# Kernel optimization log

Hardware: AMD Instinct MI355X
Metric: run time of the kernel (lower is better)

Reference implementation:

```python
import jax, jax.numpy as jnp
import numpy as np

D_MODEL = 256
N_HEADS = 8
HEAD_DIM = D_MODEL // N_HEADS  # 32
N_LEVELS = 4
N_POINTS = 4
LEVEL_SHAPES = [(100, 100), (50, 50), (25, 25), (13, 13)]
LEVEL_STARTS = [0] + list(np.cumsum([h * w for h, w in LEVEL_SHAPES]))[:-1]
LEN_IN = int(sum(h * w for h, w in LEVEL_SHAPES))  # 13294
BATCH = 2
LEN_Q = LEN_IN  # encoder self-attention


def _offset_bias():
    # faithful to MSDeformAttn._reset_parameters for sampling_offsets bias
    thetas = np.arange(N_HEADS, dtype=np.float32) * (2.0 * np.pi / N_HEADS)
    grid = np.stack([np.cos(thetas), np.sin(thetas)], -1)
    grid = grid / np.abs(grid).max(-1, keepdims=True)
    grid = np.tile(grid.reshape(N_HEADS, 1, 1, 2), (1, N_LEVELS, N_POINTS, 1))
    for i in range(N_POINTS):
        grid[:, :, i, :] *= i + 1
    return jnp.asarray(grid.reshape(-1), dtype=jnp.float32)


def setup_inputs() -> dict:
    key = jax.random.key(0)
    ks = jax.random.split(key, 10)
    s = 1.0 / np.sqrt(D_MODEL)
    inp = {
        "query": jax.random.normal(ks[0], (BATCH, LEN_Q, D_MODEL), jnp.float32),
        "reference_points": jax.random.uniform(ks[1], (BATCH, LEN_Q, N_LEVELS, 2), jnp.float32),
        "input_flatten": jax.random.normal(ks[2], (BATCH, LEN_IN, D_MODEL), jnp.float32),
        "input_spatial_shapes": jnp.asarray(LEVEL_SHAPES, dtype=jnp.int32),
        "W_value": jax.random.normal(ks[3], (D_MODEL, D_MODEL), jnp.float32) * s,
        "b_value": jnp.zeros((D_MODEL,), jnp.float32),
        "W_off": jax.random.normal(ks[4], (D_MODEL, N_HEADS * N_LEVELS * N_POINTS * 2), jnp.float32) * 0.01,
        "b_off": _offset_bias(),
        "W_attn": jax.random.normal(ks[5], (D_MODEL, N_HEADS * N_LEVELS * N_POINTS), jnp.float32) * 0.01,
        "b_attn": jnp.zeros((N_HEADS * N_LEVELS * N_POINTS,), jnp.float32),
        "W_out": jax.random.normal(ks[6], (D_MODEL, D_MODEL), jnp.float32) * s,
        "b_out": jnp.zeros((D_MODEL,), jnp.float32),
    }
    return inp


def _corner(v_t, ix, iy, h, w):
    # v_t: (n, M, h*w, D); ix/iy: (n, M, LqP) int32. Zero padding outside.
    valid = (ix >= 0) & (ix < w) & (iy >= 0) & (iy < h)
    idx = jnp.clip(iy, 0, h - 1) * w + jnp.clip(ix, 0, w - 1)
    g = jnp.take_along_axis(v_t, idx[..., None], axis=2)  # (n, M, LqP, D)
    return g * valid[..., None].astype(v_t.dtype)


def _ms_deform_attn(query, reference_points, input_flatten,
                    W_value, b_value, W_off, b_off, W_attn, b_attn, W_out, b_out):
    n, lq, _ = query.shape
    value = (input_flatten @ W_value + b_value).reshape(n, LEN_IN, N_HEADS, HEAD_DIM)
    offs = (query @ W_off + b_off).reshape(n, lq, N_HEADS, N_LEVELS, N_POINTS, 2)
    aw = jax.nn.softmax(
        (query @ W_attn + b_attn).reshape(n, lq, N_HEADS, N_LEVELS * N_POINTS), axis=-1
    ).reshape(n, lq, N_HEADS, N_LEVELS, N_POINTS)
    # offset_normalizer = (w, h) per level
    norm = jnp.asarray([[w, h] for h, w in LEVEL_SHAPES], dtype=query.dtype)
    loc = reference_points[:, :, None, :, None, :] + offs / norm[None, None, None, :, None, :]

    acc = jnp.zeros((n, N_HEADS, lq, HEAD_DIM), dtype=value.dtype)
    for l, (h, w) in enumerate(LEVEL_SHAPES):
        s0 = LEVEL_STARTS[l]
        v_t = jnp.transpose(value[:, s0:s0 + h * w], (0, 2, 1, 3))  # (n, M, hw, D)
        ll = loc[:, :, :, l]  # (n, lq, M, P, 2) in [0,1]
        # grid_sample bilinear, align_corners=False: pixel = coord*size - 0.5
        x = ll[..., 0] * w - 0.5
        y = ll[..., 1] * h - 0.5
        x0 = jnp.floor(x); y0 = jnp.floor(y)
        tx = x - x0; ty = y - y0
        ix0 = x0.astype(jnp.int32); iy0 = y0.astype(jnp.int32)
        flat = lambda a: jnp.transpose(a, (0, 2, 1, 3)).reshape(n, N_HEADS, lq * N_POINTS)
        ix0f, iy0f = flat(ix0), flat(iy0)
        txf = flat(tx)[..., None]; tyf = flat(ty)[..., None]
        g00 = _corner(v_t, ix0f, iy0f, h, w)
        g01 = _corner(v_t, ix0f + 1, iy0f, h, w)
        g10 = _corner(v_t, ix0f, iy0f + 1, h, w)
        g11 = _corner(v_t, ix0f + 1, iy0f + 1, h, w)
        samp = (g00 * (1 - txf) * (1 - tyf) + g01 * txf * (1 - tyf)
                + g10 * (1 - txf) * tyf + g11 * txf * tyf)
        samp = samp.reshape(n, N_HEADS, lq, N_POINTS, HEAD_DIM)
        wl = jnp.transpose(aw[:, :, :, l], (0, 2, 1, 3))[..., None]  # (n, M, lq, P, 1)
        acc = acc + (samp * wl).sum(axis=3)

    out = jnp.transpose(acc, (0, 2, 1, 3)).reshape(n, lq, D_MODEL)
    return out @ W_out + b_out


def reference(query, reference_points, input_flatten, input_spatial_shapes,
              W_value, b_value, W_off, b_off, W_attn, b_attn, W_out, b_out):
    # input_spatial_shapes carried for signature fidelity; level geometry is static.
    return _ms_deform_attn(query, reference_points, input_flatten,
                           W_value, b_value, W_off, b_off, W_attn, b_attn, W_out, b_out)
```

## Files before the change

### kernel.cpp

```cpp
#include <hip/hip_runtime.h>

#define NH 8
#define HD 32
#define NL 4
#define NP 4
#define DM 256
#define LEN_IN_C 13294
#define LQ_C 13294
#define B_C 2
#define M_TOTAL (B_C * LQ_C)
#define MT_TILES 1662
#define GQ 32
#define QBLKS 831
#define LROWB 1040

typedef __attribute__((ext_vector_type(8))) short short8;
typedef __attribute__((ext_vector_type(4))) float floatx4;

__device__ __forceinline__ unsigned short f2bf(float x) {
    union { float f; unsigned int u; } a; a.f = x;
    unsigned int r = (a.u + 0x7FFFu + ((a.u >> 16) & 1u)) >> 16;
    return (unsigned short)r;
}
__device__ __forceinline__ unsigned short f2h(float x) {
    unsigned int r;
    asm("v_cvt_f16_f32 %0, %1" : "=v"(r) : "v"(x));
    return (unsigned short)r;
}
__device__ __forceinline__ unsigned int cvtpk_bf16(float lo, float hi) {
    unsigned int r;
    asm("v_cvt_pk_bf16_f32 %0, %1, %2" : "=v"(r) : "v"(lo), "v"(hi));
    return r;
}

#define FMAMIX_LO(acc, v, w) \
    asm("v_fma_mix_f32 %0, %1, %2, %0 op_sel_hi:[1,0,0]" : "+v"(acc) : "v"(v), "v"(w))
#define FMAMIX_HI(acc, v, w) \
    asm("v_fma_mix_f32 %0, %1, %2, %0 op_sel:[1,0,0] op_sel_hi:[1,0,0]" : "+v"(acc) : "v"(v), "v"(w))

__device__ __forceinline__ void dma16(const float* g, float* l) {
    __builtin_amdgcn_global_load_lds(
        (const __attribute__((address_space(1))) unsigned int*)(g),
        (__attribute__((address_space(3))) unsigned int*)(l), 16, 0, 0);
}

__device__ __forceinline__ void conv_b_body(const float* __restrict__ W,
                                            unsigned short* __restrict__ Bsw,
                                            int Nsrc, int NTsrc, int NTtotal, int ntOff,
                                            int vblk) {
    const int u = vblk * 256 + threadIdx.x;
    const int lane = u & 63;
    const int unit = u >> 6;
    const int ntl = unit % NTsrc;
    const int kc = unit / NTsrc;
    const int n = ntl * 16 + (lane & 15);
    const int k0 = kc * 32 + (lane >> 4) * 8;
    short8 v;
#pragma unroll
    for (int j = 0; j < 8; ++j)
        v[j] = (short)f2bf(W[(size_t)(k0 + j) * Nsrc + n]);
    ((short8*)Bsw)[(size_t)(kc * NTtotal + ntOff + ntl) * 64 + lane] = v;
}

__global__ __launch_bounds__(256) void conv_weights_kernel(const float* __restrict__ Wv,
                                                           const float* __restrict__ Woff,
                                                           const float* __restrict__ Wattn,
                                                           const float* __restrict__ Wout,
                                                           const float* __restrict__ boff,
                                                           const float* __restrict__ battn,
                                                           unsigned short* __restrict__ BswV,
                                                           unsigned short* __restrict__ BswOA,
                                                           unsigned short* __restrict__ BswO,
                                                           float* __restrict__ fbias,
                                                           unsigned short* __restrict__ value,
                                                           unsigned short* __restrict__ AccSw) {
    const int blk = blockIdx.x;
    if (blk < 32)        conv_b_body(Wv,    BswV,  256, 16, 16, 0,  blk);
    else if (blk < 64)   conv_b_body(Woff,  BswOA, 256, 16, 24, 0,  blk - 32);
    else if (blk < 80)   conv_b_body(Wattn, BswOA, 128,  8, 24, 16, blk - 64);
    else if (blk < 112)  conv_b_body(Wout,  BswO,  256, 16, 16, 0,  blk - 80);
    else if (blk < 114) {
        const int t = (blk - 112) * 256 + threadIdx.x;
        if (t < 384) fbias[t] = (t < 256) ? boff[t] : battn[t - 256];
        else if (t < 416) {
            const int j = t - 384;
            value[-32 + j] = 0;
            value[(size_t)M_TOTAL * 256 + j] = 0;
        }
    } else {
        const int idx = threadIdx.x;
        if (idx < 128) {
            const int kc = idx >> 4;
            const int sub = idx & 15;
            const int lane = (12 + (sub & 3)) + 16 * (sub >> 2);
            const size_t unit = (size_t)(1661 * 8 + kc) * 64 + lane;
            short8 z = (short8){0, 0, 0, 0, 0, 0, 0, 0};
            ((short8*)AccSw)[unit] = z;
        }
    }
}

template <int NT, int OUTMODE>
__device__ __forceinline__ void tile_compute_f32lds(const float* __restrict__ sA,
                                                    const unsigned short* __restrict__ Bsw,
                                                    const float* __restrict__ bias,
                                                    void* __restrict__ Cout, int M, int trow,
                                                    int lane, int wave) {
    constexpr int NTW = NT / 4;
    const int m = lane & 15;
    const int q = lane >> 4;
    const short8* Bu = (const short8*)Bsw;

    floatx4 acc[NTW];
#pragma unroll
    for (int t = 0; t < NTW; ++t) acc[t] = (floatx4){0.f, 0.f, 0.f, 0.f};

#pragma unroll 2
    for (int kc = 0; kc < 8; ++kc) {
        const char* fb = (const char*)sA + m * LROWB + kc * 128 + q * 32;
        const float4 f0 = *(const float4*)fb;
        const float4 f1 = *(const float4*)(fb + 16);
        union { uint4 u; short8 s; } c;
        c.u.x = cvtpk_bf16(f0.x, f0.y); c.u.y = cvtpk_bf16(f0.z, f0.w);
        c.u.z = cvtpk_bf16(f1.x, f1.y); c.u.w = cvtpk_bf16(f1.z, f1.w);
        const short8 a = c.s;
#pragma unroll
        for (int t = 0; t < NTW; ++t) {
            const short8 b = Bu[(size_t)(kc * NT + wave * NTW + t) * 64 + lane];
            acc[t] = __builtin_amdgcn_mfma_f32_16x16x32_bf16(a, b, acc[t], 0, 0, 0);
        }
    }

    const int N = NT * 16;
    const int colq = lane & 15;
    const int rowq = (lane >> 4) * 4;
#pragma unroll
    for (int t = 0; t < NTW; ++t) {
        const int col = (wave * NTW + t) * 16 + colq;
        const float bc = bias[col];
#pragma unroll
        for (int reg = 0; reg < 4; ++reg) {
            const int row = trow + rowq + reg;
            if (row < M) {
                const float v = acc[t][reg] + bc;
                if (OUTMODE == 1) {
                    const int bb = row >= LEN_IN_C;
                    const int pos = row - (bb ? LEN_IN_C : 0);
                    const int hh = col >> 5;
                    const int dd = col & 31;
                    ((unsigned short*)Cout)[((size_t)((bb << 3) + hh) * LEN_IN_C + pos) * 32 + dd] = f2h(v);
                } else {
                    ((float*)Cout)[(size_t)row * N + col] = v;
                }
            }
        }
    }
}

__global__ __launch_bounds__(256) void front_gemm_kernel(const float* __restrict__ inflat,
                                                         const float* __restrict__ query,
                                                         const unsigned short* __restrict__ BswV,
                                                         const unsigned short* __restrict__ BswOA,
                                                         const float* __restrict__ bv,
                                                         const float* __restrict__ fbias,
                                                         unsigned short* __restrict__ value,
                                                         float* __restrict__ fused, int M) {
    __shared__ float sA[16 * LROWB / 4];
    const int tid = threadIdx.x;
    const int lane = tid & 63;
    const int wave = tid >> 6;
    const int x = blockIdx.x;
    const int flavor = x & 1;
    const int trow = (x >> 1) * 16;
    const float* A = flavor ? query : inflat;

#pragma unroll
    for (int i = 0; i < 4; ++i) {
        const int lrow = i * 4 + wave;
        const int srow = min(trow + lrow, M - 1);
        dma16(A + (size_t)srow * 256 + lane * 4,
              (float*)((char*)sA + lrow * LROWB));
    }
    __syncthreads();

    if (flavor == 0)
        tile_compute_f32lds<16, 1>(sA, BswV, bv, (void*)value, M, trow, lane, wave);
    else
        tile_compute_f32lds<24, 0>(sA, BswOA, fbias, (void*)fused, M, trow, lane, wave);
}

__global__ __launch_bounds__(256) void back_gemm_kernel(const unsigned short* __restrict__ Asw,
                                                        const unsigned short* __restrict__ Bsw,
                                                        const float* __restrict__ bias,
                                                        float* __restrict__ Cout, int M) {
    const int tid = threadIdx.x;
    const int lane = tid & 63;
    const int wave = tid >> 6;
    const int x = blockIdx.x;
    const int rt = x >> 1;
    const int half = x & 1;
    const int nt0 = half * 8 + wave * 2;

    const short8* Au = (const short8*)Asw;
    const short8* Bu = (const short8*)Bsw;

    floatx4 acc[2];
    acc[0] = (floatx4){0.f, 0.f, 0.f, 0.f};
    acc[1] = acc[0];

#pragma unroll 2
    for (int kc = 0; kc < 8; ++kc) {
        const short8 a = Au[(size_t)(rt * 8 + kc) * 64 + lane];
#pragma unroll
        for (int t = 0; t < 2; ++t) {
            const short8 b = Bu[(size_t)(kc * 16 + nt0 + t) * 64 + lane];
            acc[t] = __builtin_amdgcn_mfma_f32_16x16x32_bf16(a, b, acc[t], 0, 0, 0);
        }
    }

    const int colq = lane & 15;
    const int rowq = (lane >> 4) * 4;
#pragma unroll
    for (int t = 0; t < 2; ++t) {
        const int col = (nt0 + t) * 16 + colq;
        const float bc = bias[col];
#pragma unroll
        for (int reg = 0; reg < 4; ++reg) {
            const int row = rt * 16 + rowq + reg;
            if (row < M)
                Cout[(size_t)row * 256 + col] = acc[t][reg] + bc;
        }
    }
}

__global__ __launch_bounds__(256, 8) void msda_sample_kernel(const float* __restrict__ refp,
                                                             const unsigned short* __restrict__ value,
                                                             const float* __restrict__ fused,
                                                             unsigned short* __restrict__ AccSw) {
    constexpr int lvl_hw[4] = {100, 50, 25, 13};
    constexpr int lvl_s[4] = {0, 10000, 12500, 13125};

    const int wg = blockIdx.x;
    const int h = wg & 7;
    const int q0 = (wg >> 3) * GQ;
    const int tid = threadIdx.x;

    __shared__ float s_ref[GQ * 8];
    __shared__ uint4 s_pd[2][GQ * 17];

    s_ref[tid] = refp[min(q0 * 8 + tid, M_TOTAL * 8 - 1)];
    __syncthreads();

#pragma unroll
    for (int jj = 0; jj < 2; ++jj) {
        const int job = jj * 256 + tid;
        const int qq = job >> 4;
        const int t16 = job & 15;
        const int l = t16 >> 2;
        const int bq = min(q0 + qq, M_TOTAL - 1);
        const int b = (bq >= LQ_C) ? 1 : 0;

        const float logit = fused[(size_t)bq * 384 + 256 + h * 16 + t16];
        float m = logit;
#pragma unroll
        for (int mask = 1; mask < 16; mask <<= 1) m = fmaxf(m, __shfl_xor(m, mask));
        const float e = __expf(logit - m);
        float s = e;
#pragma unroll
        for (int mask = 1; mask < 16; mask <<= 1) s += __shfl_xor(s, mask);
        const float aw = e / s;

        const int whl = lvl_hw[l];
        const float fwh = (float)whl;
        const float2 oxy = *(const float2*)(fused + (size_t)bq * 384 + (h * 16 + t16) * 2);
        const float x = s_ref[qq * 8 + l * 2] * fwh + oxy.x - 0.5f;
        const float y = s_ref[qq * 8 + l * 2 + 1] * fwh + oxy.y - 0.5f;
        const float x0f = floorf(x), y0f = floorf(y);
        const float tx = x - x0f, ty = y - y0f;
        const int ix0 = (int)x0f, iy0 = (int)y0f;

        const bool xv0 = (unsigned)ix0 < (unsigned)whl;
        const bool xv1 = (unsigned)(ix0 + 1) < (unsigned)whl;
        const bool yv0 = (unsigned)iy0 < (unsigned)whl;
        const bool yv1 = (unsigned)(iy0 + 1) < (unsigned)whl;

        const int cxp = min(max(ix0, -1), whl - 1);
        const int cy0 = min(max(iy0, 0), whl - 1);
        const int cy1 = min(max(iy0 + 1, 0), whl - 1);

        const int posb = (b * 8 + h) * LEN_IN_C + lvl_s[l];
        const int offT = (posb + cy0 * whl + cxp) * 64;
        const int offB = (posb + cy1 * whl + cxp) * 64;
        const float w00 = (xv0 && yv0) ? aw * (1.f - tx) * (1.f - ty) : 0.f;
        const float w01 = (xv1 && yv0) ? aw * tx * (1.f - ty) : 0.f;
        const float w10 = (xv0 && yv1) ? aw * (1.f - tx) * ty : 0.f;
        const float w11 = (xv1 && yv1) ? aw * tx * ty : 0.f;
        const int slot = qq * 17 + t16;
        uint4 d0, d1;
        d0.x = (unsigned)offT; d0.y = (unsigned)offB;
        d0.z = __float_as_uint(w00); d0.w = __float_as_uint(w10);
        d1.x = (unsigned)offT; d1.y = (unsigned)offB;
        d1.z = __float_as_uint(w01); d1.w = __float_as_uint(w11);
        s_pd[0][slot] = d0;
        s_pd[1][slot] = d1;
    }
    __syncthreads();

    const int qq = tid >> 3;
    const int l8 = tid & 7;
    const char* vbp = (const char*)value + l8 * 16;
    const int pbase = qq * 17;
    const int side = (l8 >> 2) & 1;

    float a0 = 0.f, a1 = 0.f, a2 = 0.f, a3 = 0.f;
    float a4 = 0.f, a5 = 0.f, a6 = 0.f, a7 = 0.f;
#pragma unroll 2
    for (int pt = 0; pt < 16; ++pt) {
        const uint4 d = s_pd[side][pbase + pt];
        const float wt = __uint_as_float(d.z);
        const float wb = __uint_as_float(d.w);
        const uint4 vt = *(const uint4*)(vbp + (int)d.x);
        const uint4 vb = *(const uint4*)(vbp + (int)d.y);
        FMAMIX_LO(a0, vt.x, wt); FMAMIX_HI(a1, vt.x, wt);
        FMAMIX_LO(a2, vt.y, wt); FMAMIX_HI(a3, vt.y, wt);
        FMAMIX_LO(a4, vt.z, wt); FMAMIX_HI(a5, vt.z, wt);
        FMAMIX_LO(a6, vt.w, wt); FMAMIX_HI(a7, vt.w, wt);
        FMAMIX_LO(a0, vb.x, wb); FMAMIX_HI(a1, vb.x, wb);
        FMAMIX_LO(a2, vb.y, wb); FMAMIX_HI(a3, vb.y, wb);
        FMAMIX_LO(a4, vb.z, wb); FMAMIX_HI(a5, vb.z, wb);
        FMAMIX_LO(a6, vb.w, wb); FMAMIX_HI(a7, vb.w, wb);
    }

    a0 += __shfl_xor(a0, 4); a1 += __shfl_xor(a1, 4);
    a2 += __shfl_xor(a2, 4); a3 += __shfl_xor(a3, 4);
    a4 += __shfl_xor(a4, 4); a5 += __shfl_xor(a5, 4);
    a6 += __shfl_xor(a6, 4); a7 += __shfl_xor(a7, 4);

    const int bq = q0 + qq;
    if (side == 0 && bq < M_TOTAL) {
        const int rt = bq >> 4, mm = bq & 15;
        const int unit = (rt * 8 + h) * 64 + ((l8 & 3) * 16 + mm);
        uint4 o;
        o.x = cvtpk_bf16(a0, a1);
        o.y = cvtpk_bf16(a2, a3);
        o.z = cvtpk_bf16(a4, a5);
        o.w = cvtpk_bf16(a6, a7);
        *(uint4*)(AccSw + (size_t)unit * 8) = o;
    }
}

extern "C" void kernel_launch(void* const* d_in, const int* in_sizes, int n_in,
                              void* d_out, int out_size, void* d_ws, size_t ws_size,
                              hipStream_t stream) {
    const float* query  = (const float*)d_in[0];
    const float* refp   = (const float*)d_in[1];
    const float* inflat = (const float*)d_in[2];
    const float* Wv    = (const float*)d_in[4];
    const float* bv    = (const float*)d_in[5];
    const float* Woff  = (const float*)d_in[6];
    const float* boff  = (const float*)d_in[7];
    const float* Wattn = (const float*)d_in[8];
    const float* battn = (const float*)d_in[9];
    const float* Wout  = (const float*)d_in[10];
    const float* bout  = (const float*)d_in[11];
    float* out = (float*)d_out;

    char* p = (char*)d_ws;
    unsigned short* AccSw = (unsigned short*)p;
    p += (size_t)MT_TILES * 8 * 64 * 8 * sizeof(unsigned short);
    unsigned short* BswV = (unsigned short*)p;   p += (size_t)8 * 16 * 64 * 8 * 2;
    unsigned short* BswOA = (unsigned short*)p;  p += (size_t)8 * 24 * 64 * 8 * 2;
    unsigned short* BswO = (unsigned short*)p;   p += (size_t)8 * 16 * 64 * 8 * 2;
    float* fbias = (float*)p;                    p += 384 * sizeof(float);
    unsigned short* value = (unsigned short*)p + 32;
    p += ((size_t)M_TOTAL * 256 + 64) * sizeof(unsigned short);
    float* fused = (float*)p;                    p += (size_t)M_TOTAL * 384 * 4;

    const int M = M_TOTAL;

    conv_weights_kernel<<<115, 256, 0, stream>>>(Wv, Woff, Wattn, Wout, boff, battn,
                                                 BswV, BswOA, BswO, fbias, value, AccSw);
    front_gemm_kernel<<<MT_TILES * 2, 256, 0, stream>>>(inflat, query, BswV, BswOA,
                                                        bv, fbias, value, fused, M);
    msda_sample_kernel<<<QBLKS * 8, 256, 0, stream>>>(refp, value, fused, AccSw);
    back_gemm_kernel<<<MT_TILES * 2, 256, 0, stream>>>(AccSw, BswO, bout, out, M);
}
```

Before: 196.1 us.

## Fuse offset/attention projection GEMM into the sampling kernel per head

Moves the query projection for sampling offsets and attention logits out of the front GEMM and into the sampling kernel. Each block loads its 32 query rows, converts them to bf16 in LDS, and computes only its head's 48 columns with MFMA, so the fp32 'fused' intermediate buffer is no longer written to and read back from global memory. In exchange, each query row is re-read and re-converted by all 8 head blocks, LDS use per block grows, and the occupancy hint drops from 8 to 4 blocks.

Result: no change. 193.8 us (-1.2%).

```diff
diff --git a/kernel.cpp b/kernel.cpp
--- a/kernel.cpp
+++ b/kernel.cpp
@@ -66,26 +66,38 @@
                                                            const float* __restrict__ Woff,
                                                            const float* __restrict__ Wattn,
                                                            const float* __restrict__ Wout,
-                                                           const float* __restrict__ boff,
-                                                           const float* __restrict__ battn,
                                                            unsigned short* __restrict__ BswV,
-                                                           unsigned short* __restrict__ BswOA,
+                                                           unsigned short* __restrict__ BswH,
                                                            unsigned short* __restrict__ BswO,
-                                                           float* __restrict__ fbias,
                                                            unsigned short* __restrict__ value,
                                                            unsigned short* __restrict__ AccSw) {
     const int blk = blockIdx.x;
     if (blk < 32)        conv_b_body(Wv,    BswV,  256, 16, 16, 0,  blk);
-    else if (blk < 64)   conv_b_body(Woff,  BswOA, 256, 16, 24, 0,  blk - 32);
-    else if (blk < 80)   conv_b_body(Wattn, BswOA, 128,  8, 24, 16, blk - 64);
-    else if (blk < 112)  conv_b_body(Wout,  BswO,  256, 16, 16, 0,  blk - 80);
-    else if (blk < 114) {
-        const int t = (blk - 112) * 256 + threadIdx.x;
-        if (t < 384) fbias[t] = (t < 256) ? boff[t] : battn[t - 256];
-        else if (t < 416) {
-            const int j = t - 384;
-            value[-32 + j] = 0;
-            value[(size_t)M_TOTAL * 256 + j] = 0;
+    else if (blk < 80) {
+        const int u = (blk - 32) * 256 + threadIdx.x;
+        const int lane = u & 63;
+        const int unit = u >> 6;
+        const int h = unit / 24;
+        const int rem = unit % 24;
+        const int kc = rem / 3;
+        const int ntl = rem % 3;
+        const int colq = lane & 15;
+        const int k0 = kc * 32 + (lane >> 4) * 8;
+        const float* W = (ntl < 2) ? Woff : Wattn;
+        const int Nsrc = (ntl < 2) ? 256 : 128;
+        const int n = (ntl < 2) ? (h * 32 + ntl * 16 + colq) : (h * 16 + colq);
+        short8 v;
+#pragma unroll
+        for (int j = 0; j < 8; ++j)
+            v[j] = (short)f2bf(W[(size_t)(k0 + j) * Nsrc + n]);
+        ((short8*)BswH)[(size_t)unit * 64 + lane] = v;
+    }
+    else if (blk < 112)  conv_b_body(Wout, BswO, 256, 16, 16, 0, blk - 80);
+    else if (blk < 113) {
+        const int t = threadIdx.x;
+        if (t < 32) {
+            value[-32 + t] = 0;
+            value[(size_t)M_TOTAL * 256 + t] = 0;
         }
     } else {
         const int idx = threadIdx.x;
@@ -100,20 +112,32 @@
     }
 }
 
-template <int NT, int OUTMODE>
-__device__ __forceinline__ void tile_compute_f32lds(const float* __restrict__ sA,
-                                                    const unsigned short* __restrict__ Bsw,
-                                                    const float* __restrict__ bias,
-                                                    void* __restrict__ Cout, int M, int trow,
-                                                    int lane, int wave) {
-    constexpr int NTW = NT / 4;
+__global__ __launch_bounds__(256) void front_gemm_kernel(const float* __restrict__ inflat,
+                                                         const unsigned short* __restrict__ BswV,
+                                                         const float* __restrict__ bv,
+                                                         unsigned short* __restrict__ value, int M) {
+    __shared__ float sA[16 * LROWB / 4];
+    const int tid = threadIdx.x;
+    const int lane = tid & 63;
+    const int wave = tid >> 6;
+    const int trow = blockIdx.x * 16;
+
+#pragma unroll
+    for (int i = 0; i < 4; ++i) {
+        const int lrow = i * 4 + wave;
+        const int srow = min(trow + lrow, M - 1);
+        dma16(inflat + (size_t)srow * 256 + lane * 4,
+              (float*)((char*)sA + lrow * LROWB));
+    }
+    __syncthreads();
+
     const int m = lane & 15;
     const int q = lane >> 4;
-    const short8* Bu = (const short8*)Bsw;
-
-    floatx4 acc[NTW];
-#pragma unroll
-    for (int t = 0; t < NTW; ++t) acc[t] = (floatx4){0.f, 0.f, 0.f, 0.f};
+    const short8* Bu = (const short8*)BswV;
+
+    floatx4 acc[4];
+#pragma unroll
+    for (int t = 0; t < 4; ++t) acc[t] = (floatx4){0.f, 0.f, 0.f, 0.f};
 
 #pragma unroll 2
     for (int kc = 0; kc < 8; ++kc) {
@@ -125,68 +149,31 @@
         c.u.z = cvtpk_bf16(f1.x, f1.y); c.u.w = cvtpk_bf16(f1.z, f1.w);
         const short8 a = c.s;
 #pragma unroll
-        for (int t = 0; t < NTW; ++t) {
-            const short8 b = Bu[(size_t)(kc * NT + wave * NTW + t) * 64 + lane];
+        for (int t = 0; t < 4; ++t) {
+            const short8 b = Bu[(size_t)(kc * 16 + wave * 4 + t) * 64 + lane];
             acc[t] = __builtin_amdgcn_mfma_f32_16x16x32_bf16(a, b, acc[t], 0, 0, 0);
         }
     }
 
-    const int N = NT * 16;
     const int colq = lane & 15;
     const int rowq = (lane >> 4) * 4;
 #pragma unroll
-    for (int t = 0; t < NTW; ++t) {
-        const int col = (wave * NTW + t) * 16 + colq;
-        const float bc = bias[col];
+    for (int t = 0; t < 4; ++t) {
+        const int col = (wave * 4 + t) * 16 + colq;
+        const float bc = bv[col];
 #pragma unroll
         for (int reg = 0; reg < 4; ++reg) {
             const int row = trow + rowq + reg;
             if (row < M) {
                 const float v = acc[t][reg] + bc;
-                if (OUTMODE == 1) {
-                    const int bb = row >= LEN_IN_C;
-                    const int pos = row - (bb ? LEN_IN_C : 0);
-                    const int hh = col >> 5;
-                    const int dd = col & 31;
-                    ((unsigned short*)Cout)[((size_t)((bb << 3) + hh) * LEN_IN_C + pos) * 32 + dd] = f2h(v);
-                } else {
-                    ((float*)Cout)[(size_t)row * N + col] = v;
-                }
+                const int bb = row >= LEN_IN_C;
+                const int pos = row - (bb ? LEN_IN_C : 0);
+                const int hh = col >> 5;
+                const int dd = col & 31;
+                value[((size_t)((bb << 3) + hh) * LEN_IN_C + pos) * 32 + dd] = f2h(v);
             }
         }
     }
-}
-
-__global__ __launch_bounds__(256) void front_gemm_kernel(const float* __restrict__ inflat,
-                                                         const float* __restrict__ query,
-                                                         const unsigned short* __restrict__ BswV,
-                                                         const unsigned short* __restrict__ BswOA,
-                                                         const float* __restrict__ bv,
-                                                         const float* __restrict__ fbias,
-                                                         unsigned short* __restrict__ value,
-                                                         float* __restrict__ fused, int M) {
-    __shared__ float sA[16 * LROWB / 4];
-    const int tid = threadIdx.x;
-    const int lane = tid & 63;
-    const int wave = tid >> 6;
-    const int x = blockIdx.x;
-    const int flavor = x & 1;
-    const int trow = (x >> 1) * 16;
-    const float* A = flavor ? query : inflat;
-
-#pragma unroll
-    for (int i = 0; i < 4; ++i) {
-        const int lrow = i * 4 + wave;
-        const int srow = min(trow + lrow, M - 1);
-        dma16(A + (size_t)srow * 256 + lane * 4,
-              (float*)((char*)sA + lrow * LROWB));
-    }
-    __syncthreads();
-
-    if (flavor == 0)
-        tile_compute_f32lds<16, 1>(sA, BswV, bv, (void*)value, M, trow, lane, wave);
-    else
-        tile_compute_f32lds<24, 0>(sA, BswOA, fbias, (void*)fused, M, trow, lane, wave);
 }
 
 __global__ __launch_bounds__(256) void back_gemm_kernel(const unsigned short* __restrict__ Asw,
@@ -233,10 +220,13 @@
     }
 }
 
-__global__ __launch_bounds__(256, 8) void msda_sample_kernel(const float* __restrict__ refp,
-                                                             const unsigned short* __restrict__ value,
-                                                             const float* __restrict__ fused,
-                                                             unsigned short* __restrict__ AccSw) {
+__global__ __launch_bounds__(256, 4) void msda_fused_kernel(const float* __restrict__ refp,
+                                                            const float* __restrict__ query,
+                                                            const unsigned short* __restrict__ value,
+                                                            const unsigned short* __restrict__ BswH,
+                                                            const float* __restrict__ boff,
+                                                            const float* __restrict__ battn,
+                                                            unsigned short* __restrict__ AccSw) {
     constexpr int lvl_hw[4] = {100, 50, 25, 13};
     constexpr int lvl_s[4] = {0, 10000, 12500, 13125};
 
@@ -244,11 +234,59 @@
     const int h = wg & 7;
     const int q0 = (wg >> 3) * GQ;
     const int tid = threadIdx.x;
+    const int lane = tid & 63;
+    const int wave = tid >> 6;
 
     __shared__ float s_ref[GQ * 8];
-    __shared__ uint4 s_pd[2][GQ * 17];
+    __shared__ float s_fused[GQ][50];
+    __shared__ __attribute__((aligned(16))) char s_mix[17408];
+    uint4* s_pdb = (uint4*)s_mix;
 
     s_ref[tid] = refp[min(q0 * 8 + tid, M_TOTAL * 8 - 1)];
+
+#pragma unroll
+    for (int i = 0; i < 8; ++i) {
+        const int li = i * 1024 + tid * 4;
+        const int lrow = li >> 8;
+        const int lcol = li & 255;
+        const int srow = min(q0 + lrow, M_TOTAL - 1);
+        const float4 f = *(const float4*)(query + (size_t)srow * 256 + lcol);
+        uint2 pk;
+        pk.x = cvtpk_bf16(f.x, f.y);
+        pk.y = cvtpk_bf16(f.z, f.w);
+        *(uint2*)(s_mix + ((li * 2) ^ ((lrow & 7) << 4))) = pk;
+    }
+    __syncthreads();
+
+    {
+        const int m = lane & 15;
+        const int q = lane >> 4;
+        const int swz = (m & 7) << 4;
+        const short8* Bu = (const short8*)BswH;
+        const int colq = lane & 15;
+        const int rowq = (lane >> 4) * 4;
+#pragma unroll
+        for (int pass = 0; pass < 2; ++pass) {
+            const int i = wave + pass * 4;
+            if (i < 6) {
+                const int r = i & 1;
+                const int ct = i >> 1;
+                floatx4 acc = (floatx4){0.f, 0.f, 0.f, 0.f};
+#pragma unroll
+                for (int kc = 0; kc < 8; ++kc) {
+                    const short8 a = *(const short8*)(s_mix +
+                        (((m + r * 16) * 512 + kc * 64 + q * 16) ^ swz));
+                    const short8 b = Bu[(size_t)(h * 24 + kc * 3 + ct) * 64 + lane];
+                    acc = __builtin_amdgcn_mfma_f32_16x16x32_bf16(a, b, acc, 0, 0, 0);
+                }
+                const float bc = (ct < 2) ? boff[h * 32 + ct * 16 + colq]
+                                          : battn[h * 16 + colq];
+#pragma unroll
+                for (int reg = 0; reg < 4; ++reg)
+                    s_fused[r * 16 + rowq + reg][ct * 16 + colq] = acc[reg] + bc;
+            }
+        }
+    }
     __syncthreads();
 
 #pragma unroll
@@ -260,7 +298,7 @@
         const int bq = min(q0 + qq, M_TOTAL - 1);
         const int b = (bq >= LQ_C) ? 1 : 0;
 
-        const float logit = fused[(size_t)bq * 384 + 256 + h * 16 + t16];
+        const float logit = s_fused[qq][32 + t16];
         float m = logit;
 #pragma unroll
         for (int mask = 1; mask < 16; mask <<= 1) m = fmaxf(m, __shfl_xor(m, mask));
@@ -272,9 +310,10 @@
 
         const int whl = lvl_hw[l];
         const float fwh = (float)whl;
-        const float2 oxy = *(const float2*)(fused + (size_t)bq * 384 + (h * 16 + t16) * 2);
-        const float x = s_ref[qq * 8 + l * 2] * fwh + oxy.x - 0.5f;
-        const float y = s_ref[qq * 8 + l * 2 + 1] * fwh + oxy.y - 0.5f;
+        const float ox = s_fused[qq][t16 * 2];
+        const float oy = s_fused[qq][t16 * 2 + 1];
+        const float x = s_ref[qq * 8 + l * 2] * fwh + ox - 0.5f;
+        const float y = s_ref[qq * 8 + l * 2 + 1] * fwh + oy - 0.5f;
         const float x0f = floorf(x), y0f = floorf(y);
         const float tx = x - x0f, ty = y - y0f;
         const int ix0 = (int)x0f, iy0 = (int)y0f;
@@ -301,22 +340,22 @@
         d0.z = __float_as_uint(w00); d0.w = __float_as_uint(w10);
         d1.x = (unsigned)offT; d1.y = (unsigned)offB;
         d1.z = __float_as_uint(w01); d1.w = __float_as_uint(w11);
-        s_pd[0][slot] = d0;
-        s_pd[1][slot] = d1;
+        s_pdb[slot] = d0;
+        s_pdb[GQ * 17 + slot] = d1;
     }
     __syncthreads();
 
     const int qq = tid >> 3;
     const int l8 = tid & 7;
     const char* vbp = (const char*)value + l8 * 16;
-    const int pbase = qq * 17;
     const int side = (l8 >> 2) & 1;
+    const uint4* pd = s_pdb + side * (GQ * 17) + qq * 17;
 
     float a0 = 0.f, a1 = 0.f, a2 = 0.f, a3 = 0.f;
     float a4 = 0.f, a5 = 0.f, a6 = 0.f, a7 = 0.f;
 #pragma unroll 2
     for (int pt = 0; pt < 16; ++pt) {
-        const uint4 d = s_pd[side][pbase + pt];
+        const uint4 d = pd[pt];
         const float wt = __uint_as_float(d.z);
         const float wb = __uint_as_float(d.w);
         const uint4 vt = *(const uint4*)(vbp + (int)d.x);
@@ -369,19 +408,17 @@
     unsigned short* AccSw = (unsigned short*)p;
     p += (size_t)MT_TILES * 8 * 64 * 8 * sizeof(unsigned short);
     unsigned short* BswV = (unsigned short*)p;   p += (size_t)8 * 16 * 64 * 8 * 2;
-    unsigned short* BswOA = (unsigned short*)p;  p += (size_t)8 * 24 * 64 * 8 * 2;
+    unsigned short* BswH = (unsigned short*)p;   p += (size_t)192 * 64 * 8 * 2;
     unsigned short* BswO = (unsigned short*)p;   p += (size_t)8 * 16 * 64 * 8 * 2;
-    float* fbias = (float*)p;                    p += 384 * sizeof(float);
     unsigned short* value = (unsigned short*)p + 32;
     p += ((size_t)M_TOTAL * 256 + 64) * sizeof(unsigned short);
-    float* fused = (float*)p;                    p += (size_t)M_TOTAL * 384 * 4;
 
     const int M = M_TOTAL;
 
-    conv_weights_kernel<<<115, 256, 0, stream>>>(Wv, Woff, Wattn, Wout, boff, battn,
-                                                 BswV, BswOA, BswO, fbias, value, AccSw);
-    front_gemm_kernel<<<MT_TILES * 2, 256, 0, stream>>>(inflat, query, BswV, BswOA,
-                                                        bv, fbias, value, fused, M);
-    msda_sample_kernel<<<QBLKS * 8, 256, 0, stream>>>(refp, value, fused, AccSw);
+    conv_weights_kernel<<<114, 256, 0, stream>>>(Wv, Woff, Wattn, Wout,
+                                                 BswV, BswH, BswO, value, AccSw);
+    front_gemm_kernel<<<MT_TILES, 256, 0, stream>>>(inflat, BswV, bv, value, M);
+    msda_fused_kernel<<<QBLKS * 8, 256, 0, stream>>>(refp, query, value, BswH,
+                                                     boff, battn, AccSw);
     back_gemm_kernel<<<MT_TILES * 2, 256, 0, stream>>>(AccSw, BswO, bout, out, M);
 }
```
